# Kernel tuning notes

Measured on AMD Instinct MI355X. Metric: run time of the kernel, lower is better.

## Reference

```python
import jax, jax.numpy as jnp
import numpy as np

N_NODES = 100000
N_EDGES = 1600000
IN_DIM = 128
OUT_DIM = 32
NUM_HEADS = 4


def setup_inputs() -> dict:
    key = jax.random.key(0)
    k1, k2, k3, k4, k5, k6 = jax.random.split(key, 6)
    feat = jax.random.normal(k1, (N_NODES, IN_DIM), dtype=jnp.float32)
    # xavier-uniform-ish scales
    fc_w = jax.random.normal(k2, (OUT_DIM * NUM_HEADS, IN_DIM), dtype=jnp.float32) * (1.0 / np.sqrt(IN_DIM))
    attn_src = jax.random.normal(k3, (1, NUM_HEADS, OUT_DIM), dtype=jnp.float32) * 0.1
    attn_dst = jax.random.normal(k4, (1, NUM_HEADS, OUT_DIM), dtype=jnp.float32) * 0.1
    src = jax.random.randint(k5, (N_EDGES,), 0, N_NODES, dtype=jnp.int64)
    dst = jax.random.randint(k6, (N_EDGES,), 0, N_NODES, dtype=jnp.int64)
    return {"feat": feat, "fc_w": fc_w, "attn_src": attn_src, "attn_dst": attn_dst, "src": src, "dst": dst}


def reference(feat, fc_w, attn_src, attn_dst, src, dst):
    N = feat.shape[0]
    # fc: [N, H*D] -> [N, H, D]
    h = (feat @ fc_w.T).reshape(N, NUM_HEADS, OUT_DIM)
    # per-node attention logits [N, H]
    e_src = jnp.sum(h * attn_src, axis=-1)
    e_dst = jnp.sum(h * attn_dst, axis=-1)
    # per-edge logits, LeakyReLU(0.2)  [E, H]
    e = e_src[src] + e_dst[dst]
    e = jnp.where(e > 0, e, 0.2 * e)
    # edge softmax over incoming edges of each dst node
    m = jax.ops.segment_max(e, dst, num_segments=N)          # [N, H], -inf for empty
    a = jnp.exp(e - m[dst])                                  # [E, H]
    s = jax.ops.segment_sum(a, dst, num_segments=N)          # [N, H]
    a = a / jnp.where(s[dst] > 0, s[dst], 1.0)
    # weighted scatter-sum aggregation: u_mul_e + sum
    msg = h[src] * a[:, :, None]                             # [E, H, D]
    out = jax.ops.segment_sum(msg, dst, num_segments=N)      # [N, H, D]
    h_out = out.reshape(N, NUM_HEADS * OUT_DIM)
    # residual: in_dim == out_dim*num_heads -> identity residual
    return h_out + feat
```

## Files before the change

kernel.cpp:

```cpp
#include <hip/hip_runtime.h>

#define HD 128
#define NHEADS 4
#define MBLK 128
#define APITCH 136

#define CHUNK_SHIFT 8
#define MAXCH 512
#define CLCAP 4352
#define PT_EDGES 2048
#define EPT 8
#define SUB_SHIFT 6
#define SUBN 64
#define CAP 48

#define H8_SCALE   15.875f
#define H8_INVSCALE 0.062992126f

typedef __attribute__((ext_vector_type(8))) short bf16x8;
typedef __attribute__((ext_vector_type(4))) float f32x4;

__device__ __forceinline__ unsigned short f2bf(float x) {
    union { float f; unsigned u; } a; a.f = x;
    unsigned r = a.u + 0x7fffu + ((a.u >> 16) & 1u);
    return (unsigned short)(r >> 16);
}

__global__ __launch_bounds__(256) void partition_edges(
    const int* __restrict__ src, const int* __restrict__ dst,
    int* __restrict__ cursor,
    int2* __restrict__ clist,
    int2* __restrict__ spillP, int* __restrict__ nspillP,
    int E, int nchunks, int spillPCap)
{
    __shared__ int lcnt[MAXCH];
    __shared__ int gbase[MAXCH];
    __shared__ unsigned short rnk[PT_EDGES];
    const int tid = threadIdx.x;
    for (int i = tid; i < MAXCH; i += 256) lcnt[i] = 0;
    __syncthreads();

    const int ebase = blockIdx.x * PT_EDGES;

#pragma unroll
    for (int k = 0; k < EPT; k++) {
        int idx = tid + k * 256;
        int e = ebase + idx;
        if (e < E) {
            int d = dst[e];
            rnk[idx] = (unsigned short)atomicAdd(&lcnt[d >> CHUNK_SHIFT], 1);
        }
    }
    __syncthreads();

    for (int c = tid; c < nchunks; c += 256) {
        int cnt = lcnt[c];
        gbase[c] = cnt ? atomicAdd(&cursor[c], cnt) : 0;
    }
    __syncthreads();

#pragma unroll
    for (int k = 0; k < EPT; k++) {
        int idx = tid + k * 256;
        int e = ebase + idx;
        if (e < E) {
            int d = dst[e], s = src[e];
            int c = d >> CHUNK_SHIFT;
            int pos = gbase[c] + (int)rnk[idx];
            if (pos < CLCAP) {
                clist[(size_t)c * CLCAP + pos] = make_int2(d, s);
            } else {
                int kk = atomicAdd(nspillP, 1);
                if (kk < spillPCap) spillP[kk] = make_int2(d, s);
            }
        }
    }
}

__global__ __launch_bounds__(256, 2) void gemm_mfma(
    const float* __restrict__ feat, const float* __restrict__ fc_w,
    const float* __restrict__ attn_src, const float* __restrict__ attn_dst,
    signed char* __restrict__ h8, float* __restrict__ e_src, float* __restrict__ e_dst,
    int N)
{
    __shared__ unsigned short As[MBLK * APITCH];
    __shared__ unsigned short Bs[HD * APITCH];
    const int tid = threadIdx.x;
    const int row0 = blockIdx.x * MBLK;

    for (int i = tid; i < 128 * 32; i += 256) {
        int o = i >> 5, j = i & 31;
        float4 v = ((const float4*)fc_w)[i];
        ushort4 u; u.x = f2bf(v.x); u.y = f2bf(v.y); u.z = f2bf(v.z); u.w = f2bf(v.w);
        *(ushort4*)&Bs[o * APITCH + j * 4] = u;
    }
    for (int i = tid; i < MBLK * 32; i += 256) {
        int r = i >> 5, j = i & 31;
        int rowg = row0 + r;
        float4 v = make_float4(0.f, 0.f, 0.f, 0.f);
        if (rowg < N) {
            v = ((const float4*)feat)[(size_t)rowg * 32 + j];
        }
        ushort4 u; u.x = f2bf(v.x); u.y = f2bf(v.y); u.z = f2bf(v.z); u.w = f2bf(v.w);
        *(ushort4*)&As[r * APITCH + j * 4] = u;
    }
    __syncthreads();

    const int w = tid >> 6, lane = tid & 63, quad = lane >> 4, lr = lane & 15;
    f32x4 acc[2][8];
#pragma unroll
    for (int rt = 0; rt < 2; rt++)
#pragma unroll
        for (int ct = 0; ct < 8; ct++) acc[rt][ct] = (f32x4){0.f, 0.f, 0.f, 0.f};

#pragma unroll
    for (int ks = 0; ks < 4; ks++) {
        const int k0 = ks * 32 + quad * 8;
        bf16x8 a0 = *(const bf16x8*)&As[(w * 32 + lr) * APITCH + k0];
        bf16x8 a1 = *(const bf16x8*)&As[(w * 32 + 16 + lr) * APITCH + k0];
        bf16x8 bf[8];
#pragma unroll
        for (int ct = 0; ct < 8; ct++)
            bf[ct] = *(const bf16x8*)&Bs[(ct * 16 + lr) * APITCH + k0];
#pragma unroll
        for (int ct = 0; ct < 8; ct++) {
            acc[0][ct] = __builtin_amdgcn_mfma_f32_16x16x32_bf16(a0, bf[ct], acc[0][ct], 0, 0, 0);
            acc[1][ct] = __builtin_amdgcn_mfma_f32_16x16x32_bf16(a1, bf[ct], acc[1][ct], 0, 0, 0);
        }
    }

#pragma unroll
    for (int rt = 0; rt < 2; rt++) {
#pragma unroll
        for (int ct = 0; ct < 8; ct++) {
            int col = ct * 16 + lr;
#pragma unroll
            for (int reg = 0; reg < 4; reg++) {
                int row = row0 + w * 32 + rt * 16 + quad * 4 + reg;
                if (row < N) {
                    float v = acc[rt][ct][reg];
                    v = fminf(fmaxf(v, -8.f), 8.f);
                    int q = (int)rintf(v * H8_SCALE);
                    h8[(size_t)row * 128 + col] = (signed char)q;
                }
            }
        }
    }

    float as_v[8], ad_v[8];
#pragma unroll
    for (int ct = 0; ct < 8; ct++) {
        as_v[ct] = attn_src[ct * 16 + lr];
        ad_v[ct] = attn_dst[ct * 16 + lr];
    }
#pragma unroll
    for (int rt = 0; rt < 2; rt++) {
#pragma unroll
        for (int reg = 0; reg < 4; reg++) {
            int row = row0 + w * 32 + rt * 16 + quad * 4 + reg;
            float ps[4], pd[4];
#pragma unroll
            for (int hd = 0; hd < 4; hd++) {
                ps[hd] = acc[rt][2 * hd][reg] * as_v[2 * hd] + acc[rt][2 * hd + 1][reg] * as_v[2 * hd + 1];
                pd[hd] = acc[rt][2 * hd][reg] * ad_v[2 * hd] + acc[rt][2 * hd + 1][reg] * ad_v[2 * hd + 1];
            }
#pragma unroll
            for (int off = 1; off < 16; off <<= 1) {
#pragma unroll
                for (int hd = 0; hd < 4; hd++) {
                    ps[hd] += __shfl_xor(ps[hd], off);
                    pd[hd] += __shfl_xor(pd[hd], off);
                }
            }
            if (lr == 0 && row < N) {
                *(float4*)&e_src[(size_t)row * 4] = make_float4(ps[0], ps[1], ps[2], ps[3]);
                *(float4*)&e_dst[(size_t)row * 4] = make_float4(pd[0], pd[1], pd[2], pd[3]);
            }
        }
    }
}

__global__ __launch_bounds__(512) void agg_chunk(
    const int2* __restrict__ clist, const int* __restrict__ cursor,
    const int2* __restrict__ spillP, const int* __restrict__ nspillP,
    const signed char* __restrict__ h8,
    const float* __restrict__ e_src, const float* __restrict__ e_dst,
    const float* __restrict__ feat, float* __restrict__ out,
    int2* __restrict__ spillB, int* __restrict__ nspillB,
    int N, int spillPCap, int spillBCap)
{
    __shared__ int bucket[SUBN][CAP];
    __shared__ int lcnt[SUBN];
    const int c = blockIdx.x;
    const int tid = threadIdx.x;
    const int nodebase = c << SUB_SHIFT;

    if (tid < SUBN) lcnt[tid] = 0;
    __syncthreads();

    const int chunkC = c >> (CHUNK_SHIFT - SUB_SHIFT);
    int cnt = cursor[chunkC]; if (cnt > CLCAP) cnt = CLCAP;
    const int2* base = clist + (size_t)chunkC * CLCAP;
    for (int i = tid; i < cnt; i += 512) {
        int2 p = base[i];
        if ((p.x >> SUB_SHIFT) == c) {
            int ln = p.x - nodebase;
            int pos = atomicAdd(&lcnt[ln], 1);
            if (pos < CAP) bucket[ln][pos] = p.y;
            else { int kk = atomicAdd(nspillB, 1); if (kk < spillBCap) spillB[kk] = p; }
        }
    }
    int nsp = *nspillP; if (nsp > spillPCap) nsp = spillPCap;
    for (int i = tid; i < nsp; i += 512) {
        int2 p = spillP[i];
        if ((p.x >> SUB_SHIFT) == c) {
            int ln = p.x - nodebase;
            int pos = atomicAdd(&lcnt[ln], 1);
            if (pos < CAP) bucket[ln][pos] = p.y;
            else { int kk = atomicAdd(nspillB, 1); if (kk < spillBCap) spillB[kk] = p; }
        }
    }
    __syncthreads();

    const int lane  = tid & 63;
    const int wid   = tid >> 6;
    const int grp8  = lane >> 3;
    const int q     = lane & 7;
    const int head  = q >> 1;

    const int ln = wid * 8 + grp8;
    const int n = nodebase + ln;
    const bool active = (n < N);
    const int deg = active ? lcnt[ln] : 0;
    int md = deg;
    md = max(md, __shfl_xor(md, 8));
    md = max(md, __shfl_xor(md, 16));
    md = max(md, __shfl_xor(md, 32));
    if (md == 0) {
        if (active) {
            const float4* f = (const float4*)(feat + (size_t)n * HD) + q * 4;
            float4* o = (float4*)(out + (size_t)n * HD) + q * 4;
#pragma unroll
            for (int k = 0; k < 4; k++) o[k] = f[k];
        }
        return;
    }
    const float ed = active ? e_dst[(size_t)n * 4 + head] : 0.f;
    const int fdeg = deg < CAP ? deg : CAP;
    const int mdc = md < CAP ? md : CAP;

    f32x4 a0 = (f32x4){0.f, 0.f, 0.f, 0.f};
    f32x4 a1 = (f32x4){0.f, 0.f, 0.f, 0.f};
    f32x4 a2 = (f32x4){0.f, 0.f, 0.f, 0.f};
    f32x4 a3 = (f32x4){0.f, 0.f, 0.f, 0.f};
    float s_l = 0.f;
#pragma unroll 4
    for (int j = 0; j < mdc; ++j) {
        float ev = 0.f; int si = 0;
        if (j < fdeg) {
            si = bucket[ln][j];
            float v = e_src[(size_t)si * 4 + head] + ed;
            v = v > 0.f ? v : 0.2f * v;
            ev = __expf(v);
        }
        s_l += ev;
        const float evs = ev * H8_INVSCALE;
        uint4 hv = *(const uint4*)&h8[(size_t)si * 128 + q * 16];
        a0.x += evs * (float)(int)(signed char)(hv.x);
        a0.y += evs * (float)(int)(signed char)(hv.x >> 8);
        a0.z += evs * (float)(int)(signed char)(hv.x >> 16);
        a0.w += evs * (float)(int)(signed char)(hv.x >> 24);
        a1.x += evs * (float)(int)(signed char)(hv.y);
        a1.y += evs * (float)(int)(signed char)(hv.y >> 8);
        a1.z += evs * (float)(int)(signed char)(hv.y >> 16);
        a1.w += evs * (float)(int)(signed char)(hv.y >> 24);
        a2.x += evs * (float)(int)(signed char)(hv.z);
        a2.y += evs * (float)(int)(signed char)(hv.z >> 8);
        a2.z += evs * (float)(int)(signed char)(hv.z >> 16);
        a2.w += evs * (float)(int)(signed char)(hv.z >> 24);
        a3.x += evs * (float)(int)(signed char)(hv.w);
        a3.y += evs * (float)(int)(signed char)(hv.w >> 8);
        a3.z += evs * (float)(int)(signed char)(hv.w >> 16);
        a3.w += evs * (float)(int)(signed char)(hv.w >> 24);
    }
    if (__any(deg > CAP)) {
        int ns = *nspillB; if (ns > spillBCap) ns = spillBCap;
        for (int k = 0; k < ns; ++k) {
            int2 p = spillB[k];
            if (active && deg > CAP && p.x == n) {
                int si = p.y;
                float v = e_src[(size_t)si * 4 + head] + ed;
                v = v > 0.f ? v : 0.2f * v;
                float ev = __expf(v);
                s_l += ev;
                const float evs = ev * H8_INVSCALE;
                uint4 hv = *(const uint4*)&h8[(size_t)si * 128 + q * 16];
                a0.x += evs * (float)(int)(signed char)(hv.x);
                a0.y += evs * (float)(int)(signed char)(hv.x >> 8);
                a0.z += evs * (float)(int)(signed char)(hv.x >> 16);
                a0.w += evs * (float)(int)(signed char)(hv.x >> 24);
                a1.x += evs * (float)(int)(signed char)(hv.y);
                a1.y += evs * (float)(int)(signed char)(hv.y >> 8);
                a1.z += evs * (float)(int)(signed char)(hv.y >> 16);
                a1.w += evs * (float)(int)(signed char)(hv.y >> 24);
                a2.x += evs * (float)(int)(signed char)(hv.z);
                a2.y += evs * (float)(int)(signed char)(hv.z >> 8);
                a2.z += evs * (float)(int)(signed char)(hv.z >> 16);
                a2.w += evs * (float)(int)(signed char)(hv.z >> 24);
                a3.x += evs * (float)(int)(signed char)(hv.w);
                a3.y += evs * (float)(int)(signed char)(hv.w >> 8);
                a3.z += evs * (float)(int)(signed char)(hv.w >> 16);
                a3.w += evs * (float)(int)(signed char)(hv.w >> 24);
            }
        }
    }
    if (active) {
        const float inv = (deg > 0) ? (1.0f / s_l) : 0.f;
        const float4* f = (const float4*)(feat + (size_t)n * HD) + q * 4;
        float4* o = (float4*)(out + (size_t)n * HD) + q * 4;
        float4 c0 = f[0], c1 = f[1], c2 = f[2], c3 = f[3];
        c0.x += a0.x * inv; c0.y += a0.y * inv; c0.z += a0.z * inv; c0.w += a0.w * inv;
        c1.x += a1.x * inv; c1.y += a1.y * inv; c1.z += a1.z * inv; c1.w += a1.w * inv;
        c2.x += a2.x * inv; c2.y += a2.y * inv; c2.z += a2.z * inv; c2.w += a2.w * inv;
        c3.x += a3.x * inv; c3.y += a3.y * inv; c3.z += a3.z * inv; c3.w += a3.w * inv;
        o[0] = c0; o[1] = c1; o[2] = c2; o[3] = c3;
    }
}

extern "C" void kernel_launch(void* const* d_in, const int* in_sizes, int n_in,
                              void* d_out, int out_size, void* d_ws, size_t ws_size,
                              hipStream_t stream) {
    const float* feat     = (const float*)d_in[0];
    const float* fc_w     = (const float*)d_in[1];
    const float* attn_src = (const float*)d_in[2];
    const float* attn_dst = (const float*)d_in[3];
    const int*   src      = (const int*)d_in[4];
    const int*   dst      = (const int*)d_in[5];
    const int N = in_sizes[0] / HD;
    const int E = in_sizes[4];
    float* out = (float*)d_out;

    const int nchunks = (N + 255) >> CHUNK_SHIFT;
    const int nsub    = (N + SUBN - 1) >> SUB_SHIFT;
    const int spillPCap = E / 8;
    const int spillBCap = E / 8;

    signed char* h8 = (signed char*)d_ws;
    float* e_src  = (float*)(h8 + (size_t)N * HD);
    float* e_dst  = e_src + (size_t)N * NHEADS;
    int* cursor   = (int*)(e_dst + (size_t)N * NHEADS);
    int* nspillP  = cursor + nchunks;
    int* nspillB  = nspillP + 1;
    int hdr = nchunks + 2;
    hdr = (hdr + 1) & ~1;
    int2* clist   = (int2*)(cursor + hdr);
    int2* spillP  = clist + (size_t)nchunks * CLCAP;
    int2* spillB  = spillP + spillPCap;

    const int npart = (E + PT_EDGES - 1) / PT_EDGES;

    hipMemsetAsync(cursor, 0, (size_t)(nchunks + 2) * sizeof(int), stream);
    partition_edges<<<npart, 256, 0, stream>>>(src, dst, cursor, clist, spillP, nspillP,
                                               E, nchunks, spillPCap);
    gemm_mfma<<<(N + MBLK - 1) / MBLK, 256, 0, stream>>>(feat, fc_w, attn_src, attn_dst,
                                                         h8, e_src, e_dst, N);
    agg_chunk<<<nsub, 512, 0, stream>>>(clist, cursor, spillP, nspillP,
                                        h8, e_src, e_dst, feat, out,
                                        spillB, nspillB, N, spillPCap, spillBCap);
}
```

Baseline: 245.3 us.

## Fuse edge partitioning into GEMM kernel and pack edge entries to 32 bits

```diff
diff --git a/kernel.cpp b/kernel.cpp
--- a/kernel.cpp
+++ b/kernel.cpp
@@ -9,7 +9,6 @@
 #define MAXCH 512
 #define CLCAP 4352
 #define PT_EDGES 2048
-#define EPT 8
 #define SUB_SHIFT 6
 #define SUBN 64
 #define CAP 48
@@ -26,67 +25,66 @@
     return (unsigned short)(r >> 16);
 }
 
-__global__ __launch_bounds__(256) void partition_edges(
-    const int* __restrict__ src, const int* __restrict__ dst,
-    int* __restrict__ cursor,
-    int2* __restrict__ clist,
-    int2* __restrict__ spillP, int* __restrict__ nspillP,
-    int E, int nchunks, int spillPCap)
-{
-    __shared__ int lcnt[MAXCH];
-    __shared__ int gbase[MAXCH];
-    __shared__ unsigned short rnk[PT_EDGES];
-    const int tid = threadIdx.x;
-    for (int i = tid; i < MAXCH; i += 256) lcnt[i] = 0;
-    __syncthreads();
-
-    const int ebase = blockIdx.x * PT_EDGES;
-
-#pragma unroll
-    for (int k = 0; k < EPT; k++) {
-        int idx = tid + k * 256;
-        int e = ebase + idx;
-        if (e < E) {
-            int d = dst[e];
-            rnk[idx] = (unsigned short)atomicAdd(&lcnt[d >> CHUNK_SHIFT], 1);
-        }
-    }
-    __syncthreads();
-
-    for (int c = tid; c < nchunks; c += 256) {
-        int cnt = lcnt[c];
-        gbase[c] = cnt ? atomicAdd(&cursor[c], cnt) : 0;
-    }
-    __syncthreads();
-
-#pragma unroll
-    for (int k = 0; k < EPT; k++) {
-        int idx = tid + k * 256;
-        int e = ebase + idx;
-        if (e < E) {
-            int d = dst[e], s = src[e];
-            int c = d >> CHUNK_SHIFT;
-            int pos = gbase[c] + (int)rnk[idx];
-            if (pos < CLCAP) {
-                clist[(size_t)c * CLCAP + pos] = make_int2(d, s);
-            } else {
-                int kk = atomicAdd(nspillP, 1);
-                if (kk < spillPCap) spillP[kk] = make_int2(d, s);
-            }
-        }
-    }
-}
-
-__global__ __launch_bounds__(256, 2) void gemm_mfma(
+__global__ __launch_bounds__(256, 2) void gemm_part(
     const float* __restrict__ feat, const float* __restrict__ fc_w,
     const float* __restrict__ attn_src, const float* __restrict__ attn_dst,
+    const int* __restrict__ src, const int* __restrict__ dst,
     signed char* __restrict__ h8, float* __restrict__ e_src, float* __restrict__ e_dst,
-    int N)
+    int* __restrict__ cursor, unsigned int* __restrict__ clist,
+    int2* __restrict__ spillP, int* __restrict__ nspillP,
+    int N, int E, int epb, int nchunks, int spillPCap)
 {
     __shared__ unsigned short As[MBLK * APITCH];
     __shared__ unsigned short Bs[HD * APITCH];
     const int tid = threadIdx.x;
     const int row0 = blockIdx.x * MBLK;
+
+    {
+        int* lcnt = (int*)As;
+        int* gbase = lcnt + MAXCH;
+        unsigned short* rnk = (unsigned short*)(gbase + MAXCH);
+        const int ebase0 = blockIdx.x * epb;
+        int eend = ebase0 + epb; if (eend > E) eend = E;
+        for (int b0 = ebase0; b0 < eend; b0 += PT_EDGES) {
+            int bend = b0 + PT_EDGES; if (bend > eend) bend = eend;
+            for (int i = tid; i < MAXCH; i += 256) lcnt[i] = 0;
+            __syncthreads();
+#pragma unroll
+            for (int k = 0; k < PT_EDGES / 256; k++) {
+                int idx = tid + k * 256;
+                int e = b0 + idx;
+                if (e < bend) {
+                    int d = dst[e];
+                    rnk[idx] = (unsigned short)atomicAdd(&lcnt[d >> CHUNK_SHIFT], 1);
+                }
+            }
+            __syncthreads();
+            for (int c = tid; c < nchunks; c += 256) {
+                int cnt = lcnt[c];
+                gbase[c] = cnt ? atomicAdd(&cursor[c], cnt) : 0;
+            }
+            __syncthreads();
+#pragma unroll
+            for (int k = 0; k < PT_EDGES / 256; k++) {
+                int idx = tid + k * 256;
+                int e = b0 + idx;
+                if (e < bend) {
+                    int d = dst[e], s = src[e];
+                    int c = d >> CHUNK_SHIFT;
+                    int pos = gbase[c] + (int)rnk[idx];
+                    if (pos < CLCAP && s < (1 << 24)) {
+                        clist[(size_t)c * CLCAP + pos] =
+                            ((unsigned)(d & (CHUNK_SHIFT == 8 ? 255 : 255)) << 24) | (unsigned)s;
+                    } else {
+                        int kk = atomicAdd(nspillP, 1);
+                        if (kk < spillPCap) spillP[kk] = make_int2(d, s);
+                    }
+                }
+            }
+            __syncthreads();
+        }
+    }
+    __syncthreads();
 
     for (int i = tid; i < 128 * 32; i += 256) {
         int o = i >> 5, j = i & 31;
@@ -181,7 +179,7 @@
 }
 
 __global__ __launch_bounds__(512) void agg_chunk(
-    const int2* __restrict__ clist, const int* __restrict__ cursor,
+    const unsigned int* __restrict__ clist, const int* __restrict__ cursor,
     const int2* __restrict__ spillP, const int* __restrict__ nspillP,
     const signed char* __restrict__ h8,
     const float* __restrict__ e_src, const float* __restrict__ e_dst,
@@ -194,20 +192,22 @@
     const int c = blockIdx.x;
     const int tid = threadIdx.x;
     const int nodebase = c << SUB_SHIFT;
+    const int sub = c & ((1 << (CHUNK_SHIFT - SUB_SHIFT)) - 1);
 
     if (tid < SUBN) lcnt[tid] = 0;
     __syncthreads();
 
     const int chunkC = c >> (CHUNK_SHIFT - SUB_SHIFT);
     int cnt = cursor[chunkC]; if (cnt > CLCAP) cnt = CLCAP;
-    const int2* base = clist + (size_t)chunkC * CLCAP;
+    const unsigned int* base = clist + (size_t)chunkC * CLCAP;
     for (int i = tid; i < cnt; i += 512) {
-        int2 p = base[i];
-        if ((p.x >> SUB_SHIFT) == c) {
-            int ln = p.x - nodebase;
+        unsigned int p = base[i];
+        int dl = (int)(p >> 24);
+        if ((dl >> SUB_SHIFT) == sub) {
+            int ln = dl & (SUBN - 1);
             int pos = atomicAdd(&lcnt[ln], 1);
-            if (pos < CAP) bucket[ln][pos] = p.y;
-            else { int kk = atomicAdd(nspillB, 1); if (kk < spillBCap) spillB[kk] = p; }
+            if (pos < CAP) bucket[ln][pos] = (int)(p & 0xFFFFFFu);
+            else { int kk = atomicAdd(nspillB, 1); if (kk < spillBCap) spillB[kk] = make_int2(nodebase + ln, (int)(p & 0xFFFFFFu)); }
         }
     }
     int nsp = *nspillP; if (nsp > spillPCap) nsp = spillPCap;
@@ -353,17 +353,19 @@
     int* nspillB  = nspillP + 1;
     int hdr = nchunks + 2;
     hdr = (hdr + 1) & ~1;
-    int2* clist   = (int2*)(cursor + hdr);
-    int2* spillP  = clist + (size_t)nchunks * CLCAP;
+    unsigned int* clist = (unsigned int*)(cursor + hdr);
+    size_t clistLen = (size_t)nchunks * CLCAP;
+    clistLen = (clistLen + 1) & ~(size_t)1;
+    int2* spillP  = (int2*)(clist + clistLen);
     int2* spillB  = spillP + spillPCap;
 
-    const int npart = (E + PT_EDGES - 1) / PT_EDGES;
+    const int G = (N + MBLK - 1) / MBLK;
+    const int epb = ((E + G - 1) / G + PT_EDGES - 1) / PT_EDGES * PT_EDGES;
 
     hipMemsetAsync(cursor, 0, (size_t)(nchunks + 2) * sizeof(int), stream);
-    partition_edges<<<npart, 256, 0, stream>>>(src, dst, cursor, clist, spillP, nspillP,
-                                               E, nchunks, spillPCap);
-    gemm_mfma<<<(N + MBLK - 1) / MBLK, 256, 0, stream>>>(feat, fc_w, attn_src, attn_dst,
-                                                         h8, e_src, e_dst, N);
+    gemm_part<<<G, 256, 0, stream>>>(feat, fc_w, attn_src, attn_dst, src, dst,
+                                     h8, e_src, e_dst, cursor, clist, spillP, nspillP,
+                                     N, E, epb, nchunks, spillPCap);
     agg_chunk<<<nsub, 512, 0, stream>>>(clist, cursor, spillP, nspillP,
                                         h8, e_src, e_dst, feat, out,
                                         spillB, nspillB, N, spillPCap, spillBCap);
```

Result: faster. 228.6 us (-6.8%).
